# Performance work log

Hardware: AMD Instinct MI355X
Metric: run time of the kernel (lower is better)

Reference implementation:

```python
import jax, jax.numpy as jnp
import numpy as np

B, S, D = 2, 2048, 2048
NH, NKV, DH = 16, 4, 128
NG = NH // NKV  # query heads per kv head


def rope_apply(x, cos, sin):
    # x: [B, H, S, DH]; cos/sin: [S, DH//2]
    x1, x2 = jnp.split(x, 2, axis=-1)
    c = cos[None, None, :, :]
    s = sin[None, None, :, :]
    return jnp.concatenate([x1 * c - x2 * s, x1 * s + x2 * c], axis=-1)


def setup_inputs() -> dict:
    key = jax.random.key(0)
    ks = jax.random.split(key, 6)
    x = jax.random.normal(ks[0], (B, S, D), dtype=jnp.float32)
    # real RoPE frequencies
    inv_freq = 1.0 / (10000.0 ** (jnp.arange(0, DH // 2, dtype=jnp.float32) * 2.0 / DH))
    angles = jnp.arange(S, dtype=jnp.float32)[:, None] * inv_freq[None, :]  # [S, DH//2]
    cos, sin = jnp.cos(angles), jnp.sin(angles)
    mask = jnp.tril(jnp.ones((S, S), dtype=bool))[None, None]  # causal [1,1,S,S]
    sc = 0.02
    Wq = jax.random.normal(ks[1], (D, NH * DH), dtype=jnp.float32) * sc
    Wk = jax.random.normal(ks[2], (D, NKV * DH), dtype=jnp.float32) * sc
    Wv = jax.random.normal(ks[3], (D, NKV * DH), dtype=jnp.float32) * sc
    Wo = jax.random.normal(ks[4], (NH * DH, D), dtype=jnp.float32) * sc
    return {"x": x, "cos": cos, "sin": sin, "mask": mask,
            "Wq": Wq, "Wk": Wk, "Wv": Wv, "Wo": Wo}


def reference(x, cos, sin, mask, Wq, Wk, Wv, Wo):
    b, s, _ = x.shape
    q = (x @ Wq).reshape(b, s, NH, DH).transpose(0, 2, 1, 3)    # [B,NH,S,DH]
    k = (x @ Wk).reshape(b, s, NKV, DH).transpose(0, 2, 1, 3)   # [B,NKV,S,DH]
    v = (x @ Wv).reshape(b, s, NKV, DH).transpose(0, 2, 1, 3)
    q = rope_apply(q, cos, sin)
    k = rope_apply(k, cos, sin)
    new_kv_cache = (k, v)
    k_exp = jnp.repeat(k, NG, axis=1)  # [B,NH,S,DH]
    v_exp = jnp.repeat(v, NG, axis=1)
    scale = jnp.float32(np.sqrt(DH))
    scores = jnp.einsum('bhqd,bhkd->bhqk', q, k_exp) / scale
    scores = jnp.where(mask, scores, jnp.float32(-1e9))
    weights = jax.nn.softmax(scores, axis=-1)
    context = jnp.einsum('bhqk,bhkd->bhqd', weights, v_exp)
    context = context.transpose(0, 2, 1, 3).reshape(b, s, NH * DH)
    output = context @ Wo
    return output, new_kv_cache[0], new_kv_cache[1]
```

## Files before the change

kernel.cpp:

```cpp
#include <hip/hip_runtime.h>
#include <stdint.h>

#define Bb 2
#define Ss 2048
#define Dd 2048
#define NHh 16
#define NKVv 4
#define DHh 128
#define Mm_ (Bb*Ss)
#define NQq (NHh*DHh)

using bf16x8 = __attribute__((ext_vector_type(8))) __bf16;
using f32x4  = __attribute__((ext_vector_type(4))) float;

__device__ __forceinline__ unsigned short f2bf(float f) {
  unsigned u = __float_as_uint(f);
  u += 0x7fffu + ((u >> 16) & 1u);
  return (unsigned short)(u >> 16);
}
__device__ __forceinline__ float bf2f(unsigned short s) {
  return __uint_as_float(((unsigned)s) << 16);
}

__global__ void k_convert(const float* __restrict__ in, unsigned short* __restrict__ out, int n4) {
  const int i = blockIdx.x * blockDim.x + threadIdx.x;
  if (i >= n4) return;
  const float4 v = ((const float4*)in)[i];
  ushort4 o;
  o.x = f2bf(v.x); o.y = f2bf(v.y); o.z = f2bf(v.z); o.w = f2bf(v.w);
  ((ushort4*)out)[i] = o;
}

__global__ __launch_bounds__(256) void k_transpose(const float* __restrict__ in,
                                                   unsigned short* __restrict__ out,
                                                   int Kk, int Nn) {
  __shared__ float tile[32][33];
  const int n0 = blockIdx.x * 32, k0 = blockIdx.y * 32;
  const int tx = threadIdx.x & 31, ty = threadIdx.x >> 5;
  #pragma unroll
  for (int i = 0; i < 4; ++i)
    tile[ty + i * 8][tx] = in[(size_t)(k0 + ty + i * 8) * Nn + n0 + tx];
  __syncthreads();
  #pragma unroll
  for (int i = 0; i < 4; ++i)
    out[(size_t)(n0 + ty + i * 8) * Kk + k0 + tx] = f2bf(tile[tx][ty + i * 8]);
}

__global__ __launch_bounds__(512) void k_gemm_qkv(const unsigned short* __restrict__ A,
                                                  const unsigned short* __restrict__ BT,
                                                  unsigned short* __restrict__ Qo,
                                                  float* __restrict__ Ko,
                                                  float* __restrict__ Vo) {
  __shared__ unsigned short lds[2][2][16384];
  const int Kdim = Dd;
  const int tid = threadIdx.x;
  const int lane = tid & 63;
  const int lg = lane >> 4, ll = lane & 15;
  const int wid = tid >> 6;
  const int wm = wid >> 2, wn = wid & 3;
  const int m0 = blockIdx.y << 8, n0 = blockIdx.x << 8;

  f32x4 acc[8][4] = {};
  bf16x8 bfr[4];

  auto stage_shot = [&](int buf, int kt, int s) {
    const int c = ((s & 3) << 9) + tid;
    const int row = c >> 3, c16 = c & 7;
    const int csrc = (c16 ^ (row & 7)) << 3;
    if (s < 4) {
      const unsigned short* src = A + (size_t)(m0 + row) * Kdim + kt * 64 + csrc;
      __builtin_amdgcn_global_load_lds(
          (const __attribute__((address_space(1))) void*)src,
          (__attribute__((address_space(3))) void*)(&lds[buf][0][0] + c * 8), 16, 0, 0);
    } else {
      const unsigned short* src = BT + (size_t)(n0 + row) * Kdim + kt * 64 + csrc;
      __builtin_amdgcn_global_load_lds(
          (const __attribute__((address_space(1))) void*)src,
          (__attribute__((address_space(3))) void*)(&lds[buf][1][0] + c * 8), 16, 0, 0);
    }
  };

  #pragma unroll
  for (int s = 0; s < 8; ++s) stage_shot(0, 0, s);
  __syncthreads();

  const int nkt = Kdim >> 6;
  int cur = 0;
  for (int kt = 0; kt < nkt; ++kt) {
    const int nxt = cur ^ 1;
    const bool hn = (kt + 1 < nkt);
    const char* Atl = (const char*)&lds[cur][0][0];
    const char* Btl = (const char*)&lds[cur][1][0];

    auto rdB = [&](int ks) {
      #pragma unroll
      for (int i = 0; i < 4; ++i) {
        const int r = wn * 64 + i * 16 + ll;
        bfr[i] = *(const bf16x8*)(const void*)(
            Btl + r * 128 + ((ks * 64 + lg * 16) ^ ((r & 7) << 4)));
      }
    };
    auto quad = [&](int mh, int ks) {
      bf16x8 af[4];
      #pragma unroll
      for (int i = 0; i < 4; ++i) {
        const int r = wm * 128 + (mh * 4 + i) * 16 + ll;
        af[i] = *(const bf16x8*)(const void*)(
            Atl + r * 128 + ((ks * 64 + lg * 16) ^ ((r & 7) << 4)));
      }
      __builtin_amdgcn_s_setprio(1);
      #pragma unroll
      for (int i = 0; i < 4; ++i)
        #pragma unroll
        for (int n = 0; n < 4; ++n)
          acc[mh * 4 + i][n] =
              __builtin_amdgcn_mfma_f32_16x16x32_bf16(af[i], bfr[n], acc[mh * 4 + i][n], 0, 0, 0);
      __builtin_amdgcn_s_setprio(0);
    };

    rdB(0);
    if (hn) { stage_shot(nxt, kt + 1, 0); stage_shot(nxt, kt + 1, 1);
              stage_shot(nxt, kt + 1, 2); stage_shot(nxt, kt + 1, 3); }
    __builtin_amdgcn_s_barrier();
    quad(0, 0);
    __builtin_amdgcn_s_barrier();
    if (hn) { stage_shot(nxt, kt + 1, 4); stage_shot(nxt, kt + 1, 5);
              stage_shot(nxt, kt + 1, 6); stage_shot(nxt, kt + 1, 7); }
    __builtin_amdgcn_s_barrier();
    quad(1, 0);
    __builtin_amdgcn_s_barrier();
    rdB(1);
    __builtin_amdgcn_s_barrier();
    quad(0, 1);
    __builtin_amdgcn_s_barrier();
    quad(1, 1);
    if (hn) {
      asm volatile("s_waitcnt vmcnt(0)" ::: "memory");
    }
    __builtin_amdgcn_s_barrier();
    cur ^= 1;
  }

  #pragma unroll
  for (int mi = 0; mi < 8; ++mi)
    #pragma unroll
    for (int ni = 0; ni < 4; ++ni) {
      const int row = m0 + wm * 128 + mi * 16 + lg * 4;
      const int col = n0 + wn * 64 + ni * 16 + ll;
      #pragma unroll
      for (int jj = 0; jj < 4; ++jj) {
        if (n0 < 2048)      Qo[(size_t)(row + jj) * 2048 + col] = f2bf(acc[mi][ni][jj]);
        else if (n0 < 2560) Ko[(size_t)(row + jj) * 512 + col - 2048] = acc[mi][ni][jj];
        else                Vo[(size_t)(row + jj) * 512 + col - 2560] = acc[mi][ni][jj];
      }
    }
}

__global__ __launch_bounds__(256) void k_gemm_bt(const unsigned short* __restrict__ A,
                                                 const unsigned short* __restrict__ BT,
                                                 float* __restrict__ Cf,
                                                 int Nn, int Kk) {
  __shared__ unsigned short As[4096];
  __shared__ unsigned short Bs[4096];
  const int tid = threadIdx.x, wid = tid >> 6, lane = tid & 63;
  const int lg = lane >> 4, ll = lane & 15;
  const int wm = wid >> 1, wn = wid & 1;
  const int m0 = blockIdx.y << 7, n0 = blockIdx.x << 7;
  f32x4 acc[4][4] = {};
  const int nk = Kk >> 5;
  for (int kk = 0; kk < nk; ++kk) {
    const int k0 = kk << 5;
    __syncthreads();
    #pragma unroll
    for (int i = 0; i < 2; ++i) {
      const int call = wid * 2 + i;
      const int c = call * 64 + lane;
      const int row = c >> 2, ce = (c & 3) * 8;
      const unsigned short* ga = A  + (size_t)(m0 + row) * Kk + k0 + ce;
      const unsigned short* gb = BT + (size_t)(n0 + row) * Kk + k0 + ce;
      __builtin_amdgcn_global_load_lds(
          (const __attribute__((address_space(1))) void*)ga,
          (__attribute__((address_space(3))) void*)(As + call * 512), 16, 0, 0);
      __builtin_amdgcn_global_load_lds(
          (const __attribute__((address_space(1))) void*)gb,
          (__attribute__((address_space(3))) void*)(Bs + call * 512), 16, 0, 0);
    }
    __syncthreads();
    bf16x8 af[4], bfr[4];
    #pragma unroll
    for (int rb = 0; rb < 4; ++rb)
      af[rb] = *(const bf16x8*)(const void*)(As + (wm * 64 + rb * 16 + ll) * 32 + lg * 8);
    #pragma unroll
    for (int cb = 0; cb < 4; ++cb)
      bfr[cb] = *(const bf16x8*)(const void*)(Bs + (wn * 64 + cb * 16 + ll) * 32 + lg * 8);
    #pragma unroll
    for (int rb = 0; rb < 4; ++rb)
      #pragma unroll
      for (int cb = 0; cb < 4; ++cb)
        acc[rb][cb] = __builtin_amdgcn_mfma_f32_16x16x32_bf16(af[rb], bfr[cb], acc[rb][cb], 0, 0, 0);
  }
  #pragma unroll
  for (int rb = 0; rb < 4; ++rb)
    #pragma unroll
    for (int cb = 0; cb < 4; ++cb) {
      const int row = m0 + wm * 64 + rb * 16 + lg * 4;
      const int col = n0 + wn * 64 + cb * 16 + ll;
      #pragma unroll
      for (int jj = 0; jj < 4; ++jj)
        Cf[(size_t)(row + jj) * Nn + col] = acc[rb][cb][jj];
    }
}

__global__ void k_rope_k(const float* __restrict__ kf, const float* __restrict__ cosT,
                         const float* __restrict__ sinT, float* __restrict__ outK,
                         unsigned short* __restrict__ kbb) {
  const int idx = blockIdx.x * blockDim.x + threadIdx.x;
  if (idx >= Mm_ * NKVv * 64) return;
  const int dh2 = idx & 63;
  const int kv = (idx >> 6) & 3;
  const int m = idx >> 8;
  const int s = m & (Ss - 1);
  const int b = m >> 11;
  const size_t src = (size_t)m * 512 + kv * DHh + dh2;
  const float x1 = kf[src], x2 = kf[src + 64];
  const float c = cosT[s * 64 + dh2], sn = sinT[s * 64 + dh2];
  const float o1 = x1 * c - x2 * sn, o2 = x1 * sn + x2 * c;
  const size_t dst = ((size_t)(b * NKVv + kv) * Ss + s) * DHh + dh2;
  outK[dst] = o1; outK[dst + 64] = o2;
  kbb[dst] = f2bf(o1); kbb[dst + 64] = f2bf(o2);
}

__global__ void k_v_post(const float* __restrict__ vf, float* __restrict__ outV,
                         unsigned short* __restrict__ vTb) {
  const int idx = blockIdx.x * blockDim.x + threadIdx.x;
  if (idx >= Mm_ * NKVv * DHh) return;
  const int dh = idx & 127;
  const int kv = (idx >> 7) & 3;
  const int m = idx >> 9;
  const int s = m & (Ss - 1);
  const int b = m >> 11;
  const float v = vf[(size_t)m * 512 + kv * DHh + dh];
  outV[((size_t)(b * NKVv + kv) * Ss + s) * DHh + dh] = v;
  vTb[((size_t)(b * NKVv + kv) * DHh + dh) * Ss + s] = f2bf(v);
}

__global__ __launch_bounds__(256) void k_attn(const unsigned short* __restrict__ qb,
                                              const unsigned short* __restrict__ kb,
                                              const unsigned short* __restrict__ vT,
                                              const float* __restrict__ cosT,
                                              const float* __restrict__ sinT,
                                              unsigned short* __restrict__ ctxb) {
  const int linear = blockIdx.y * 32 + blockIdx.x;
  const int r = linear >> 8;
  const int u = linear & 255;
  const int q2 = u & 7;
  const int bh = u >> 3;
  int qt;
  if      (r == 0) qt = q2;
  else if (r == 1) qt = 15 - q2;
  else if (r == 2) qt = 16 + q2;
  else             qt = 31 - q2;

  const int b = bh >> 4, h = bh & 15;
  const int kvh = h >> 2;
  const int tid = threadIdx.x, wid = tid >> 6, lane = tid & 63;
  const int lg = lane >> 4, ll = lane & 15;
  __shared__ unsigned short kts[8192];
  __shared__ unsigned short vts[8192];
  __shared__ unsigned short p_s[4096];
  const char* ktc = (const char*)kts;
  const char* vtc = (const char*)vts;
  char* pwc = (char*)p_s + wid * 2048;
  const int swz = (ll & 7) << 4;
  const unsigned short* kbase = kb + (size_t)(b * NKVv + kvh) * Ss * DHh;
  const unsigned short* vbase = vT + (size_t)(b * NKVv + kvh) * DHh * Ss;
  const int qrow_f = qt * 64 + wid * 16 + ll;
  const unsigned short* qrow = qb + (size_t)(b * Ss + qrow_f) * NQq + h * DHh;

  uint4 rq[4];
  #pragma unroll
  for (int ks = 0; ks < 4; ++ks)
    rq[ks] = *(const uint4*)(const void*)(qrow + ks * 32 + lg * 8);
  bf16x8 qfr[4];
  {
    const unsigned short* rqs = (const unsigned short*)rq;
    unsigned short qtmp[4][8];
    const float scq = 0.12751746595544662f;
    #pragma unroll
    for (int ksh = 0; ksh < 2; ++ksh) {
      #pragma unroll
      for (int e = 0; e < 8; ++e) {
        const int dh2 = ksh * 32 + lg * 8 + e;
        const float c = cosT[qrow_f * 64 + dh2], sn = sinT[qrow_f * 64 + dh2];
        const float x1 = bf2f(rqs[ksh * 8 + e]);
        const float x2 = bf2f(rqs[(ksh + 2) * 8 + e]);
        qtmp[ksh][e]     = f2bf((x1 * c - x2 * sn) * scq);
        qtmp[ksh + 2][e] = f2bf((x1 * sn + x2 * c) * scq);
      }
    }
    #pragma unroll
    for (int ks = 0; ks < 4; ++ks) qfr[ks] = *(const bf16x8*)(const void*)qtmp[ks];
  }

  union { unsigned int u4[4]; bf16x8 v; } onesu;
  onesu.u4[0] = onesu.u4[1] = onesu.u4[2] = onesu.u4[3] = 0x3F803F80u;
  const bf16x8 onesf = onesu.v;

  f32x4 ctx[9] = {};
  const int qr0 = qt * 64 + wid * 16 + lg * 4;
  const int nkt = qt + 1;

  auto stage_k = [&](int ktile) {
    #pragma unroll
    for (int i = 0; i < 4; ++i) {
      const int s = i * 256 + tid;
      const int krow = s >> 4, kcs = (s & 15) ^ (krow & 7);
      const unsigned short* ksrc = kbase + (size_t)(ktile * 64 + krow) * DHh + kcs * 8;
      __builtin_amdgcn_global_load_lds(
          (const __attribute__((address_space(1))) void*)ksrc,
          (__attribute__((address_space(3))) void*)(kts + (i * 256 + wid * 64) * 8), 16, 0, 0);
    }
  };
  auto stage_v = [&](int ktile) {
    #pragma unroll
    for (int i = 0; i < 4; ++i) {
      const int s = i * 256 + tid;
      const int vrow = s >> 3, vcs = (s & 7) ^ (vrow & 7);
      const unsigned short* vsrc = vbase + (size_t)vrow * Ss + ktile * 64 + vcs * 8;
      __builtin_amdgcn_global_load_lds(
          (const __attribute__((address_space(1))) void*)vsrc,
          (__attribute__((address_space(3))) void*)(vts + (i * 256 + wid * 64) * 8), 16, 0, 0);
    }
  };

  stage_k(0);
  __syncthreads();
  for (int kt = 0; kt < nkt; ++kt) {
    stage_v(kt);
    f32x4 sc[4] = {};
    __builtin_amdgcn_s_setprio(1);
    #pragma unroll
    for (int ks = 0; ks < 4; ++ks) {
      #pragma unroll
      for (int cb = 0; cb < 4; ++cb) {
        const bf16x8 kfr = *(const bf16x8*)(const void*)(
            ktc + ((cb * 16 + ll) << 8) + (((ks << 6) + (lg << 4)) ^ swz));
        sc[cb] = __builtin_amdgcn_mfma_f32_16x16x32_bf16(qfr[ks], kfr, sc[cb], 0, 0, 0);
      }
    }
    __builtin_amdgcn_s_setprio(0);
    const bool domask = (kt == qt);
    float pv[4][4];
    #pragma unroll
    for (int cb = 0; cb < 4; ++cb)
      #pragma unroll
      for (int j = 0; j < 4; ++j) {
        float s = sc[cb][j];
        if (domask && (kt * 64 + cb * 16 + ll > qr0 + j)) s = -1e30f;
        pv[cb][j] = exp2f(s - 8.656170245333781f);
      }
    #pragma unroll
    for (int cb = 0; cb < 4; ++cb)
      #pragma unroll
      for (int j = 0; j < 4; ++j) {
        const int prow = lg * 4 + j;
        *(unsigned short*)(pwc + (prow << 7) + (((cb << 5) + (ll << 1)) ^ ((prow & 7) << 4))) =
            (unsigned short)((__float_as_uint(pv[cb][j]) + 0x8000u) >> 16);
      }
    __syncthreads();
    if (kt + 1 < nkt) stage_k(kt + 1);
    __builtin_amdgcn_s_setprio(1);
    #pragma unroll
    for (int k2 = 0; k2 < 2; ++k2) {
      const bf16x8 pa = *(const bf16x8*)(const void*)(
          pwc + (ll << 7) + (((k2 << 6) + (lg << 4)) ^ swz));
      #pragma unroll
      for (int ob = 0; ob < 8; ++ob) {
        const bf16x8 vfr = *(const bf16x8*)(const void*)(
            vtc + ((ob * 16 + ll) << 7) + (((k2 << 6) + (lg << 4)) ^ swz));
        ctx[ob] = __builtin_amdgcn_mfma_f32_16x16x32_bf16(pa, vfr, ctx[ob], 0, 0, 0);
      }
      ctx[8] = __builtin_amdgcn_mfma_f32_16x16x32_bf16(pa, onesf, ctx[8], 0, 0, 0);
    }
    __builtin_amdgcn_s_setprio(0);
    __syncthreads();
  }
  #pragma unroll
  for (int j = 0; j < 4; ++j) {
    const float inv = 1.f / ctx[8][j];
    unsigned short* crow = ctxb + (size_t)(b * Ss + qr0 + j) * NQq + h * DHh;
    #pragma unroll
    for (int ob = 0; ob < 8; ++ob)
      crow[ob * 16 + ll] = f2bf(ctx[ob][j] * inv);
  }
}

extern "C" void kernel_launch(void* const* d_in, const int* in_sizes, int n_in,
                              void* d_out, int out_size, void* d_ws, size_t ws_size,
                              hipStream_t stream) {
  const float* x    = (const float*)d_in[0];
  const float* cosT = (const float*)d_in[1];
  const float* sinT = (const float*)d_in[2];
  const float* Wq   = (const float*)d_in[4];
  const float* Wk   = (const float*)d_in[5];
  const float* Wv   = (const float*)d_in[6];
  const float* Wo   = (const float*)d_in[7];
  float* out  = (float*)d_out;
  float* outK = out + (size_t)Mm_ * Dd;
  float* outV = outK + (size_t)Bb * NKVv * Ss * DHh;

  char* ws = (char*)d_ws;
  size_t off = 0;
  auto alloc = [&](size_t bytes) -> void* {
    void* p = ws + off;
    off += (bytes + 255) & ~(size_t)255;
    return p;
  };
  unsigned short* xb    = (unsigned short*)alloc((size_t)Mm_ * Dd * 2);
  unsigned short* wqkvT = (unsigned short*)alloc((size_t)3072 * Dd * 2);
  unsigned short* woT   = (unsigned short*)alloc((size_t)Dd * NQq * 2);
  unsigned short* qfb   = (unsigned short*)alloc((size_t)Mm_ * NQq * 2);
  float*          kf    = (float*)alloc((size_t)Mm_ * 512 * 4);
  float*          vf    = (float*)alloc((size_t)Mm_ * 512 * 4);
  unsigned short* kbb   = (unsigned short*)alloc((size_t)Bb * NKVv * Ss * DHh * 2);
  unsigned short* vTb   = (unsigned short*)alloc((size_t)Bb * NKVv * Ss * DHh * 2);
  unsigned short* ctxb  = (unsigned short*)alloc((size_t)Mm_ * NQq * 2);
  if (off > ws_size) return;

  k_convert<<<(Mm_ * Dd / 4 + 255) / 256, 256, 0, stream>>>(x, xb, Mm_ * Dd / 4);
  k_transpose<<<dim3(64, 64), 256, 0, stream>>>(Wq, wqkvT, Dd, Dd);
  k_transpose<<<dim3(16, 64), 256, 0, stream>>>(Wk, wqkvT + (size_t)2048 * Dd, Dd, 512);
  k_transpose<<<dim3(16, 64), 256, 0, stream>>>(Wv, wqkvT + (size_t)2560 * Dd, Dd, 512);
  k_transpose<<<dim3(64, 64), 256, 0, stream>>>(Wo, woT, Dd, Dd);
  k_gemm_qkv<<<dim3(12, 16), 512, 0, stream>>>(xb, wqkvT, qfb, kf, vf);
  k_rope_k<<<(Mm_ * NKVv * 64 + 255) / 256, 256, 0, stream>>>(kf, cosT, sinT, outK, kbb);
  k_v_post<<<(Mm_ * NKVv * DHh + 255) / 256, 256, 0, stream>>>(vf, outV, vTb);
  k_attn<<<dim3(32, 32), 256, 0, stream>>>(qfb, kbb, vTb, cosT, sinT, ctxb);
  k_gemm_bt<<<dim3(16, 32), 256, 0, stream>>>(ctxb, woT, out, Dd, NQq);
}
```

Measured before the change: 242.5 us.

## Template 256-row pipelined GEMM, reuse for output projection, fuse V post-processing

Turns the QKV GEMM into a template whose N-tile width is a parameter. QKV now runs as 256x192 tiles on 256 blocks instead of 256x256 on 192, to fill more CUs. The V epilogue is fused into that GEMM: it writes the fp32 V cache and the transposed bf16 V directly, which removes the k_v_post kernel and the fp32 V intermediate. The output projection now uses the double-buffered 512-thread 256x128 kernel instead of the simple single-buffered 128x128 one. The cost is uncoalesced strided writes for transposed V in the epilogue and fewer blocks (256 vs 512) for the output GEMM.

```diff
diff --git a/kernel.cpp b/kernel.cpp
--- a/kernel.cpp
+++ b/kernel.cpp
@@ -46,42 +46,51 @@
     out[(size_t)(n0 + ty + i * 8) * Kk + k0 + tx] = f2bf(tile[tx][ty + i * 8]);
 }
 
-__global__ __launch_bounds__(512) void k_gemm_qkv(const unsigned short* __restrict__ A,
-                                                  const unsigned short* __restrict__ BT,
-                                                  unsigned short* __restrict__ Qo,
-                                                  float* __restrict__ Ko,
-                                                  float* __restrict__ Vo) {
-  __shared__ unsigned short lds[2][2][16384];
-  const int Kdim = Dd;
+template<int BNW, int MODE>
+__global__ __launch_bounds__(512) void k_gemm256(const unsigned short* __restrict__ A,
+                                                 const unsigned short* __restrict__ BT,
+                                                 int Kdim,
+                                                 unsigned short* __restrict__ Qo,
+                                                 float* __restrict__ kfo,
+                                                 float* __restrict__ outV,
+                                                 unsigned short* __restrict__ vTb,
+                                                 float* __restrict__ Cf) {
+  __shared__ unsigned short ldsA[2][16384];
+  __shared__ unsigned short ldsB[2][4096 * BNW];
   const int tid = threadIdx.x;
   const int lane = tid & 63;
   const int lg = lane >> 4, ll = lane & 15;
   const int wid = tid >> 6;
   const int wm = wid >> 2, wn = wid & 3;
-  const int m0 = blockIdx.y << 8, n0 = blockIdx.x << 8;
-
-  f32x4 acc[8][4] = {};
-  bf16x8 bfr[4];
-
-  auto stage_shot = [&](int buf, int kt, int s) {
-    const int c = ((s & 3) << 9) + tid;
+  const int m0 = blockIdx.y << 8;
+  const int n0 = blockIdx.x * (64 * BNW);
+
+  f32x4 acc[8][BNW] = {};
+  bf16x8 bfr[BNW];
+
+  auto stage_A = [&](int buf, int kt, int s) {
+    const int c = (s << 9) + tid;
     const int row = c >> 3, c16 = c & 7;
     const int csrc = (c16 ^ (row & 7)) << 3;
-    if (s < 4) {
-      const unsigned short* src = A + (size_t)(m0 + row) * Kdim + kt * 64 + csrc;
-      __builtin_amdgcn_global_load_lds(
-          (const __attribute__((address_space(1))) void*)src,
-          (__attribute__((address_space(3))) void*)(&lds[buf][0][0] + c * 8), 16, 0, 0);
-    } else {
-      const unsigned short* src = BT + (size_t)(n0 + row) * Kdim + kt * 64 + csrc;
-      __builtin_amdgcn_global_load_lds(
-          (const __attribute__((address_space(1))) void*)src,
-          (__attribute__((address_space(3))) void*)(&lds[buf][1][0] + c * 8), 16, 0, 0);
-    }
+    const unsigned short* src = A + (size_t)(m0 + row) * Kdim + kt * 64 + csrc;
+    __builtin_amdgcn_global_load_lds(
+        (const __attribute__((address_space(1))) void*)src,
+        (__attribute__((address_space(3))) void*)(&ldsA[buf][0] + c * 8), 16, 0, 0);
   };
-
-  #pragma unroll
-  for (int s = 0; s < 8; ++s) stage_shot(0, 0, s);
+  auto stage_B = [&](int buf, int kt, int s) {
+    const int c = (s << 9) + tid;
+    const int row = c >> 3, c16 = c & 7;
+    const int csrc = (c16 ^ (row & 7)) << 3;
+    const unsigned short* src = BT + (size_t)(n0 + row) * Kdim + kt * 64 + csrc;
+    __builtin_amdgcn_global_load_lds(
+        (const __attribute__((address_space(1))) void*)src,
+        (__attribute__((address_space(3))) void*)(&ldsB[buf][0] + c * 8), 16, 0, 0);
+  };
+
+  #pragma unroll
+  for (int s = 0; s < 4; ++s) stage_A(0, 0, s);
+  #pragma unroll
+  for (int s = 0; s < BNW; ++s) stage_B(0, 0, s);
   __syncthreads();
 
   const int nkt = Kdim >> 6;
@@ -89,13 +98,13 @@
   for (int kt = 0; kt < nkt; ++kt) {
     const int nxt = cur ^ 1;
     const bool hn = (kt + 1 < nkt);
-    const char* Atl = (const char*)&lds[cur][0][0];
-    const char* Btl = (const char*)&lds[cur][1][0];
+    const char* Atl = (const char*)&ldsA[cur][0];
+    const char* Btl = (const char*)&ldsB[cur][0];
 
     auto rdB = [&](int ks) {
       #pragma unroll
-      for (int i = 0; i < 4; ++i) {
-        const int r = wn * 64 + i * 16 + ll;
+      for (int i = 0; i < BNW; ++i) {
+        const int r = wn * (16 * BNW) + i * 16 + ll;
         bfr[i] = *(const bf16x8*)(const void*)(
             Btl + r * 128 + ((ks * 64 + lg * 16) ^ ((r & 7) << 4)));
       }
@@ -112,20 +121,22 @@
       #pragma unroll
       for (int i = 0; i < 4; ++i)
         #pragma unroll
-        for (int n = 0; n < 4; ++n)
+        for (int n = 0; n < BNW; ++n)
           acc[mh * 4 + i][n] =
               __builtin_amdgcn_mfma_f32_16x16x32_bf16(af[i], bfr[n], acc[mh * 4 + i][n], 0, 0, 0);
       __builtin_amdgcn_s_setprio(0);
     };
 
     rdB(0);
-    if (hn) { stage_shot(nxt, kt + 1, 0); stage_shot(nxt, kt + 1, 1);
-              stage_shot(nxt, kt + 1, 2); stage_shot(nxt, kt + 1, 3); }
+    if (hn) { stage_A(nxt, kt + 1, 0); stage_A(nxt, kt + 1, 1);
+              stage_A(nxt, kt + 1, 2); stage_A(nxt, kt + 1, 3); }
     __builtin_amdgcn_s_barrier();
     quad(0, 0);
     __builtin_amdgcn_s_barrier();
-    if (hn) { stage_shot(nxt, kt + 1, 4); stage_shot(nxt, kt + 1, 5);
-              stage_shot(nxt, kt + 1, 6); stage_shot(nxt, kt + 1, 7); }
+    if (hn) {
+      #pragma unroll
+      for (int s = 0; s < BNW; ++s) stage_B(nxt, kt + 1, s);
+    }
     __builtin_amdgcn_s_barrier();
     quad(1, 0);
     __builtin_amdgcn_s_barrier();
@@ -144,70 +155,34 @@
   #pragma unroll
   for (int mi = 0; mi < 8; ++mi)
     #pragma unroll
-    for (int ni = 0; ni < 4; ++ni) {
-      const int row = m0 + wm * 128 + mi * 16 + lg * 4;
-      const int col = n0 + wn * 64 + ni * 16 + ll;
-      #pragma unroll
-      for (int jj = 0; jj < 4; ++jj) {
-        if (n0 < 2048)      Qo[(size_t)(row + jj) * 2048 + col] = f2bf(acc[mi][ni][jj]);
-        else if (n0 < 2560) Ko[(size_t)(row + jj) * 512 + col - 2048] = acc[mi][ni][jj];
-        else                Vo[(size_t)(row + jj) * 512 + col - 2560] = acc[mi][ni][jj];
-      }
-    }
-}
-
-__global__ __launch_bounds__(256) void k_gemm_bt(const unsigned short* __restrict__ A,
-                                                 const unsigned short* __restrict__ BT,
-                                                 float* __restrict__ Cf,
-                                                 int Nn, int Kk) {
-  __shared__ unsigned short As[4096];
-  __shared__ unsigned short Bs[4096];
-  const int tid = threadIdx.x, wid = tid >> 6, lane = tid & 63;
-  const int lg = lane >> 4, ll = lane & 15;
-  const int wm = wid >> 1, wn = wid & 1;
-  const int m0 = blockIdx.y << 7, n0 = blockIdx.x << 7;
-  f32x4 acc[4][4] = {};
-  const int nk = Kk >> 5;
-  for (int kk = 0; kk < nk; ++kk) {
-    const int k0 = kk << 5;
-    __syncthreads();
-    #pragma unroll
-    for (int i = 0; i < 2; ++i) {
-      const int call = wid * 2 + i;
-      const int c = call * 64 + lane;
-      const int row = c >> 2, ce = (c & 3) * 8;
-      const unsigned short* ga = A  + (size_t)(m0 + row) * Kk + k0 + ce;
-      const unsigned short* gb = BT + (size_t)(n0 + row) * Kk + k0 + ce;
-      __builtin_amdgcn_global_load_lds(
-          (const __attribute__((address_space(1))) void*)ga,
-          (__attribute__((address_space(3))) void*)(As + call * 512), 16, 0, 0);
-      __builtin_amdgcn_global_load_lds(
-          (const __attribute__((address_space(1))) void*)gb,
-          (__attribute__((address_space(3))) void*)(Bs + call * 512), 16, 0, 0);
-    }
-    __syncthreads();
-    bf16x8 af[4], bfr[4];
-    #pragma unroll
-    for (int rb = 0; rb < 4; ++rb)
-      af[rb] = *(const bf16x8*)(const void*)(As + (wm * 64 + rb * 16 + ll) * 32 + lg * 8);
-    #pragma unroll
-    for (int cb = 0; cb < 4; ++cb)
-      bfr[cb] = *(const bf16x8*)(const void*)(Bs + (wn * 64 + cb * 16 + ll) * 32 + lg * 8);
-    #pragma unroll
-    for (int rb = 0; rb < 4; ++rb)
-      #pragma unroll
-      for (int cb = 0; cb < 4; ++cb)
-        acc[rb][cb] = __builtin_amdgcn_mfma_f32_16x16x32_bf16(af[rb], bfr[cb], acc[rb][cb], 0, 0, 0);
-  }
-  #pragma unroll
-  for (int rb = 0; rb < 4; ++rb)
-    #pragma unroll
-    for (int cb = 0; cb < 4; ++cb) {
-      const int row = m0 + wm * 64 + rb * 16 + lg * 4;
-      const int col = n0 + wn * 64 + cb * 16 + ll;
-      #pragma unroll
-      for (int jj = 0; jj < 4; ++jj)
-        Cf[(size_t)(row + jj) * Nn + col] = acc[rb][cb][jj];
+    for (int ni = 0; ni < BNW; ++ni) {
+      const int row4 = m0 + wm * 128 + mi * 16 + lg * 4;
+      const int col = n0 + wn * (16 * BNW) + ni * 16 + ll;
+      if (MODE == 1) {
+        #pragma unroll
+        for (int jj = 0; jj < 4; ++jj)
+          Cf[(size_t)(row4 + jj) * 2048 + col] = acc[mi][ni][jj];
+      } else {
+        if (col < 2048) {
+          #pragma unroll
+          for (int jj = 0; jj < 4; ++jj)
+            Qo[(size_t)(row4 + jj) * 2048 + col] = f2bf(acc[mi][ni][jj]);
+        } else if (col < 2560) {
+          #pragma unroll
+          for (int jj = 0; jj < 4; ++jj)
+            kfo[(size_t)(row4 + jj) * 512 + (col - 2048)] = acc[mi][ni][jj];
+        } else {
+          const int kv = (col - 2560) >> 7, dh = (col - 2560) & 127;
+          const int b = row4 >> 11, s0 = row4 & 2047;
+          #pragma unroll
+          for (int jj = 0; jj < 4; ++jj)
+            outV[((size_t)(b * NKVv + kv) * Ss + s0 + jj) * DHh + dh] = acc[mi][ni][jj];
+          ushort4 pk;
+          pk.x = f2bf(acc[mi][ni][0]); pk.y = f2bf(acc[mi][ni][1]);
+          pk.z = f2bf(acc[mi][ni][2]); pk.w = f2bf(acc[mi][ni][3]);
+          *(ushort4*)&vTb[((size_t)(b * NKVv + kv) * DHh + dh) * Ss + s0] = pk;
+        }
+      }
     }
 }
 
@@ -230,20 +205,6 @@
   kbb[dst] = f2bf(o1); kbb[dst + 64] = f2bf(o2);
 }
 
-__global__ void k_v_post(const float* __restrict__ vf, float* __restrict__ outV,
-                         unsigned short* __restrict__ vTb) {
-  const int idx = blockIdx.x * blockDim.x + threadIdx.x;
-  if (idx >= Mm_ * NKVv * DHh) return;
-  const int dh = idx & 127;
-  const int kv = (idx >> 7) & 3;
-  const int m = idx >> 9;
-  const int s = m & (Ss - 1);
-  const int b = m >> 11;
-  const float v = vf[(size_t)m * 512 + kv * DHh + dh];
-  outV[((size_t)(b * NKVv + kv) * Ss + s) * DHh + dh] = v;
-  vTb[((size_t)(b * NKVv + kv) * DHh + dh) * Ss + s] = f2bf(v);
-}
-
 __global__ __launch_bounds__(256) void k_attn(const unsigned short* __restrict__ qb,
                                               const unsigned short* __restrict__ kb,
                                               const unsigned short* __restrict__ vT,
@@ -421,7 +382,6 @@
   unsigned short* woT   = (unsigned short*)alloc((size_t)Dd * NQq * 2);
   unsigned short* qfb   = (unsigned short*)alloc((size_t)Mm_ * NQq * 2);
   float*          kf    = (float*)alloc((size_t)Mm_ * 512 * 4);
-  float*          vf    = (float*)alloc((size_t)Mm_ * 512 * 4);
   unsigned short* kbb   = (unsigned short*)alloc((size_t)Bb * NKVv * Ss * DHh * 2);
   unsigned short* vTb   = (unsigned short*)alloc((size_t)Bb * NKVv * Ss * DHh * 2);
   unsigned short* ctxb  = (unsigned short*)alloc((size_t)Mm_ * NQq * 2);
@@ -432,9 +392,11 @@
   k_transpose<<<dim3(16, 64), 256, 0, stream>>>(Wk, wqkvT + (size_t)2048 * Dd, Dd, 512);
   k_transpose<<<dim3(16, 64), 256, 0, stream>>>(Wv, wqkvT + (size_t)2560 * Dd, Dd, 512);
   k_transpose<<<dim3(64, 64), 256, 0, stream>>>(Wo, woT, Dd, Dd);
-  k_gemm_qkv<<<dim3(12, 16), 512, 0, stream>>>(xb, wqkvT, qfb, kf, vf);
+  k_gemm256<3, 0><<<dim3(16, 16), 512, 0, stream>>>(
+      xb, wqkvT, Dd, qfb, kf, outV, vTb, (float*)nullptr);
   k_rope_k<<<(Mm_ * NKVv * 64 + 255) / 256, 256, 0, stream>>>(kf, cosT, sinT, outK, kbb);
-  k_v_post<<<(Mm_ * NKVv * DHh + 255) / 256, 256, 0, stream>>>(vf, outV, vTb);
   k_attn<<<dim3(32, 32), 256, 0, stream>>>(qfb, kbb, vTb, cosT, sinT, ctxb);
-  k_gemm_bt<<<dim3(16, 32), 256, 0, stream>>>(ctxb, woT, out, Dd, NQq);
-}
+  k_gemm256<2, 1><<<dim3(16, 16), 512, 0, stream>>>(
+      ctxb, woT, NQq, (unsigned short*)nullptr, (float*)nullptr,
+      (float*)nullptr, (unsigned short*)nullptr, out);
+}
```

Result: faster. 204.9 us (-15.5%).
